# Performance work log

Measured on AMD Instinct MI355X. Metric: run time of the kernel, lower is better.

Reference implementation:

```python
import jax, jax.numpy as jnp
import numpy as np

NEG_SLOPE = 0.2  # PyG GATConv leaky_relu slope


def _gat_layer(x, src, dst, W, a_src, a_dst, b, concat, num_nodes):
    # x: [N, F_in], W: [F_in, H*C], a_src/a_dst: [H, C], b: [H*C] or [C]
    H, C = a_src.shape
    h = (x @ W).reshape(num_nodes, H, C)                      # [N, H, C]
    s_src = jnp.einsum('nhc,hc->nh', h, a_src)                # [N, H]
    s_dst = jnp.einsum('nhc,hc->nh', h, a_dst)                # [N, H]
    e = jax.nn.leaky_relu(s_src[src] + s_dst[dst], NEG_SLOPE) # [E, H]
    # segment softmax over edges sharing a destination node
    m = jax.ops.segment_max(e, dst, num_segments=num_nodes)
    m = jnp.where(jnp.isfinite(m), m, 0.0)
    p = jnp.exp(e - m[dst])
    z = jax.ops.segment_sum(p, dst, num_segments=num_nodes)
    alpha = p / (z[dst] + 1e-16)                              # [E, H]
    msg = h[src] * alpha[:, :, None]                          # [E, H, C]
    out = jax.ops.segment_sum(msg, dst, num_segments=num_nodes)  # [N, H, C]
    out = out.reshape(num_nodes, H * C) if concat else out.mean(axis=1)
    return out + b


def setup_inputs() -> dict:
    key = jax.random.key(0)
    ks = jax.random.split(key, 16)
    N, E, F = 100000, 800000, 128
    H, C = 4, 32
    sc_in = 1.0 / np.sqrt(F)
    inp = {
        'x': jax.random.normal(ks[0], (N, F), jnp.float32),
        'edge_index': jax.random.randint(ks[1], (2, E), 0, N, jnp.int64),
        'W1': jax.random.normal(ks[2], (F, H * C), jnp.float32) * sc_in,
        'a_src1': jax.random.normal(ks[3], (H, C), jnp.float32),
        'a_dst1': jax.random.normal(ks[4], (H, C), jnp.float32),
        'b1': jax.random.normal(ks[5], (H * C,), jnp.float32) * 0.01,
        'W2': jax.random.normal(ks[6], (F, H * C), jnp.float32) * sc_in,
        'a_src2': jax.random.normal(ks[7], (H, C), jnp.float32),
        'a_dst2': jax.random.normal(ks[8], (H, C), jnp.float32),
        'b2': jax.random.normal(ks[9], (H * C,), jnp.float32) * 0.01,
        'W3': jax.random.normal(ks[10], (F, H * F), jnp.float32) * sc_in,
        'a_src3': jax.random.normal(ks[11], (H, F), jnp.float32),
        'a_dst3': jax.random.normal(ks[12], (H, F), jnp.float32),
        'b3': jax.random.normal(ks[13], (F,), jnp.float32) * 0.01,
    }
    return inp


def reference(x, edge_index, W1, a_src1, a_dst1, b1, W2, a_src2, a_dst2, b2,
              W3, a_src3, a_dst3, b3):
    N = x.shape[0]
    # PyG GATConv default: add self loops
    loop = jnp.arange(N, dtype=edge_index.dtype)
    src = jnp.concatenate([edge_index[0], loop])
    dst = jnp.concatenate([edge_index[1], loop])
    # conv1 (concat heads) + residual + ELU
    x1 = jax.nn.elu(_gat_layer(x, src, dst, W1, a_src1, a_dst1, b1, True, N) + x)
    # intermediate conv (concat heads) + residual + ELU
    x2 = jax.nn.elu(_gat_layer(x1, src, dst, W2, a_src2, a_dst2, b2, True, N) + x1)
    # final conv (mean over heads) + residual, no ELU
    x3 = _gat_layer(x2, src, dst, W3, a_src3, a_dst3, b3, False, N) + x2
    return x3
```

## Files before the change

### kernel.cpp

```cpp
#include <hip/hip_runtime.h>
#include <hip/hip_bf16.h>
#include <cstdint>

#define NEG_SLOPE 0.2f

typedef __bf16 bf16x8 __attribute__((ext_vector_type(8)));
typedef _Float16 half8 __attribute__((ext_vector_type(8)));
typedef float  floatx4 __attribute__((ext_vector_type(4)));

__device__ __forceinline__ float us2f(unsigned short u) {
    union { unsigned int i; float f; } c; c.i = ((unsigned int)u) << 16; return c.f;
}
__device__ __forceinline__ unsigned short f2us(float f) {
    union { float f; unsigned int i; } c; c.f = f;
    unsigned int x = c.i;
    unsigned int r = (x + 0x7fffu + ((x >> 16) & 1u)) >> 16;
    return (unsigned short)r;
}
__device__ __forceinline__ unsigned short f2h(float f) {
    union { _Float16 h; unsigned short u; } c; c.h = (_Float16)f; return c.u;
}
__device__ __forceinline__ float h2f(unsigned short u) {
    union { _Float16 h; unsigned short u; } c; c.u = u; return (float)c.h;
}
__device__ __forceinline__ float ldx(const void* p, int i, int bf) {
    return bf ? us2f(((const unsigned short*)p)[i]) : ((const float*)p)[i];
}
__device__ __forceinline__ void split2(float f, unsigned short& h, unsigned short& l) {
    h = f2us(f);
    l = f2us(f - us2f(h));
}
__device__ __forceinline__ float sel4(const float* a, int i) {
    float lo = (i & 1) ? a[1] : a[0];
    float hi = (i & 1) ? a[3] : a[2];
    return (i & 2) ? hi : lo;
}
__device__ __forceinline__ void unp8(uint4 u, float* f) {
    union { unsigned int i; float ff; } a;
    a.i = u.x << 16;          f[0] = a.ff;
    a.i = u.x & 0xffff0000u;  f[1] = a.ff;
    a.i = u.y << 16;          f[2] = a.ff;
    a.i = u.y & 0xffff0000u;  f[3] = a.ff;
    a.i = u.z << 16;          f[4] = a.ff;
    a.i = u.z & 0xffff0000u;  f[5] = a.ff;
    a.i = u.w << 16;          f[6] = a.ff;
    a.i = u.w & 0xffff0000u;  f[7] = a.ff;
}

__global__ void k_detect(const unsigned short* __restrict__ x16,
                         const unsigned int* __restrict__ ei,
                         int* __restrict__ flags) {
    if (threadIdx.x == 0 && blockIdx.x == 0) {
        int cnt = 0;
        for (int i = 0; i < 1024; ++i) {
            const unsigned short u = x16[2 * i];
            const int e = (u >> 7) & 0xFF;
            if (e < 100 || e > 160) ++cnt;
        }
        flags[0] = (cnt < 256) ? 1 : 0;
        int is64 = 1;
        for (int i = 0; i < 64; ++i)
            if (ei[2 * i + 1] != 0u) { is64 = 0; break; }
        flags[1] = is64;
    }
}

__device__ __forceinline__ int edge_at(const void* ei, int f64, long long idx) {
    if (f64) return (int)((const long long*)ei)[idx];
    return ((const int*)ei)[idx];
}

__global__ void k_hist(const void* __restrict__ ei, const int* __restrict__ flags,
                       int* __restrict__ deg, int E, int N) {
    const int f64 = flags[1];
    const int EP = E + N;
    for (int e = blockIdx.x * blockDim.x + threadIdx.x; e < EP; e += gridDim.x * blockDim.x) {
        int dst = (e < E) ? edge_at(ei, f64, (long long)E + e) : (e - E);
        atomicAdd(&deg[dst], 1);
    }
}

__global__ __launch_bounds__(1024) void k_scan_a(const int* __restrict__ deg,
                                                 int* __restrict__ coff,
                                                 int* __restrict__ part, int N) {
    __shared__ int tmp[1024];
    const int t = threadIdx.x, idx = blockIdx.x * 1024 + t;
    const int v = (idx < N) ? deg[idx] : 0;
    tmp[t] = v; __syncthreads();
    for (int s = 1; s < 1024; s <<= 1) {
        int a = (t >= s) ? tmp[t - s] : 0;
        __syncthreads(); tmp[t] += a; __syncthreads();
    }
    if (idx < N) coff[idx] = tmp[t] - v;
    if (t == 1023) part[blockIdx.x] = tmp[1023];
}

__global__ __launch_bounds__(1024) void k_scan_b(int* __restrict__ part,
                                                 int* __restrict__ coff, int nblk, int N) {
    __shared__ int tmp[1024];
    const int t = threadIdx.x;
    const int v = (t < nblk) ? part[t] : 0;
    tmp[t] = v; __syncthreads();
    for (int s = 1; s < 1024; s <<= 1) {
        int a = (t >= s) ? tmp[t - s] : 0;
        __syncthreads(); tmp[t] += a; __syncthreads();
    }
    if (t < nblk) part[t] = tmp[t] - v;
    if (t == 1023) coff[N] = tmp[1023];
}

__global__ __launch_bounds__(1024) void k_scan_c(int* __restrict__ coff,
                                                 const int* __restrict__ part, int N) {
    const int idx = blockIdx.x * 1024 + threadIdx.x;
    if (idx < N) coff[idx] += part[blockIdx.x];
}

__global__ void k_scatter(const void* __restrict__ ei, const int* __restrict__ flags,
                          const int* __restrict__ coff, int* __restrict__ cpos,
                          int* __restrict__ csrc, int E, int N) {
    const int f64 = flags[1];
    const int EP = E + N;
    for (int e = blockIdx.x * blockDim.x + threadIdx.x; e < EP; e += gridDim.x * blockDim.x) {
        int src, dst;
        if (e < E) { src = edge_at(ei, f64, e); dst = edge_at(ei, f64, (long long)E + e); }
        else       { src = dst = e - E; }
        const int p = atomicAdd(&cpos[dst], 1);
        csrc[coff[dst] + p] = src;
    }
}

template <int F16>
__global__ void k_wfrag(const void* __restrict__ Wv, const int* __restrict__ flags,
                        int wstride, int total,
                        unsigned short* __restrict__ outH, unsigned short* __restrict__ outL) {
    const int bf = flags[0];
    for (int tid = blockIdx.x * blockDim.x + threadIdx.x; tid < total;
         tid += gridDim.x * blockDim.x) {
        const int j    = tid & 7;
        const int lane = (tid >> 3) & 63;
        const int ks   = (tid >> 9) & 3;
        const int ntg  = (tid >> 11) & 7;
        const int blk  = tid >> 14;
        const int k = ks * 32 + (lane >> 4) * 8 + j;
        const int c = blk * 128 + ntg * 16 + (lane & 15);
        const float v = ldx(Wv, k * wstride + c, bf);
        unsigned short h, l;
        if (F16) {
            h = f2h(v);
            l = f2h(v - h2f(h));
        } else {
            split2(v, h, l);
        }
        outH[tid] = h; outL[tid] = l;
    }
}

__global__ void k_wa(const void* __restrict__ W, const void* __restrict__ as,
                     const void* __restrict__ ad, const int* __restrict__ flags,
                     float* __restrict__ va) {
    const int bf = flags[0];
    const int t = blockIdx.x * blockDim.x + threadIdx.x;
    if (t >= 512) return;
    const int k = t >> 2, h = t & 3;
    float ss = 0.f, dd = 0.f;
    for (int c = 0; c < 128; ++c) {
        const float w = ldx(W, k * 512 + h * 128 + c, bf);
        ss = fmaf(w, ldx(as, h * 128 + c, bf), ss);
        dd = fmaf(w, ldx(ad, h * 128 + c, bf), dd);
    }
    va[k * 8 + h] = ss;
    va[k * 8 + 4 + h] = dd;
}

template <bool XRAW, int SC>
__global__ __launch_bounds__(256) void k_gemm(const void* __restrict__ Xv,
                                              const unsigned short* __restrict__ whfB,
                                              const unsigned short* __restrict__ wlfB,
                                              unsigned short* __restrict__ Y16, int ystride,
                                              float* __restrict__ ssrc,
                                              float* __restrict__ sdst,
                                              const void* __restrict__ a_src,
                                              const void* __restrict__ a_dst,
                                              const int* __restrict__ flags,
                                              int N) {
    __shared__ __align__(16) unsigned short Ah[64][136], Al[64][136];
    __shared__ float sred[2][4][SC ? 64 : 1];
    const int bf   = flags[0];
    const int t    = threadIdx.x;
    const int row0 = blockIdx.x * 64;
    const int hy   = blockIdx.y;
    const unsigned short* whf = whfB + hy * 16384;
    const unsigned short* wlf = wlfB + hy * 16384;
    const int ycol0 = hy * 128;
    const int wv   = t >> 6;
    const int lane = t & 63;
    const int quad = lane >> 4;
    const int l16  = lane & 15;

#pragma unroll
    for (int it = 0; it < 8; ++it) {
        const int id = it * 256 + t;
        const int r  = id >> 5;
        const int c  = (id & 31) * 4;
        const int gr = row0 + r;
        ushort4 h4 = make_ushort4(0, 0, 0, 0), l4 = make_ushort4(0, 0, 0, 0);
        if (gr < N) {
            if (XRAW && bf) {
                h4 = *(const ushort4*)&((const unsigned short*)Xv)[(size_t)gr * 128 + c];
            } else {
                const float4 f = *(const float4*)&((const float*)Xv)[(size_t)gr * 128 + c];
                split2(f.x, h4.x, l4.x); split2(f.y, h4.y, l4.y);
                split2(f.z, h4.z, l4.z); split2(f.w, h4.w, l4.w);
            }
        }
        *(ushort4*)&Ah[r][c] = h4;
        *(ushort4*)&Al[r][c] = l4;
    }
    __syncthreads();

    floatx4 acc[4][2];
#pragma unroll
    for (int mt = 0; mt < 4; ++mt)
#pragma unroll
        for (int nt = 0; nt < 2; ++nt) acc[mt][nt] = (floatx4){0.f, 0.f, 0.f, 0.f};

#pragma unroll
    for (int ks = 0; ks < 4; ++ks) {
        const int ko = ks * 32 + quad * 8;
        bf16x8 ah[4], al[4], bh[2], bl[2];
#pragma unroll
        for (int mt = 0; mt < 4; ++mt) ah[mt] = *(const bf16x8*)&Ah[mt * 16 + l16][ko];
        if (!(XRAW && bf)) {
#pragma unroll
            for (int mt = 0; mt < 4; ++mt) al[mt] = *(const bf16x8*)&Al[mt * 16 + l16][ko];
        }
#pragma unroll
        for (int nt = 0; nt < 2; ++nt)
            bh[nt] = *(const bf16x8*)&whf[(((wv * 2 + nt) * 4 + ks) * 64 + lane) * 8];
        if (!bf) {
#pragma unroll
            for (int nt = 0; nt < 2; ++nt)
                bl[nt] = *(const bf16x8*)&wlf[(((wv * 2 + nt) * 4 + ks) * 64 + lane) * 8];
        }
#pragma unroll
        for (int mt = 0; mt < 4; ++mt)
#pragma unroll
            for (int nt = 0; nt < 2; ++nt) {
                acc[mt][nt] = __builtin_amdgcn_mfma_f32_16x16x32_bf16(ah[mt], bh[nt], acc[mt][nt], 0, 0, 0);
                if (!bf)
                    acc[mt][nt] = __builtin_amdgcn_mfma_f32_16x16x32_bf16(ah[mt], bl[nt], acc[mt][nt], 0, 0, 0);
                if (!(XRAW && bf))
                    acc[mt][nt] = __builtin_amdgcn_mfma_f32_16x16x32_bf16(al[mt], bh[nt], acc[mt][nt], 0, 0, 0);
            }
    }

    const int aBase = hy * 128 + wv * 32;
    float as_[2], ad_[2];
#pragma unroll
    for (int nt = 0; nt < 2; ++nt) {
        as_[nt] = ldx(a_src, aBase + nt * 16 + l16, bf);
        ad_[nt] = ldx(a_dst, aBase + nt * 16 + l16, bf);
    }

#pragma unroll
    for (int mt = 0; mt < 4; ++mt) {
        const int rl = mt * 16 + quad * 4;
#pragma unroll
        for (int r = 0; r < 4; ++r) {
            const int grow = row0 + rl + r;
            if (grow < N) {
#pragma unroll
                for (int nt = 0; nt < 2; ++nt)
                    Y16[(size_t)grow * ystride + ycol0 + wv * 32 + nt * 16 + l16] =
                        f2us(acc[mt][nt][r]);
            }
            float ps = acc[mt][0][r] * as_[0] + acc[mt][1][r] * as_[1];
            float pd = acc[mt][0][r] * ad_[0] + acc[mt][1][r] * ad_[1];
#pragma unroll
            for (int mk = 1; mk <= 8; mk <<= 1) {
                ps += __shfl_xor(ps, mk);
                pd += __shfl_xor(pd, mk);
            }
            if (SC == 0) {
                if (l16 == 0 && grow < N) {
                    ssrc[(size_t)grow * 4 + wv] = ps;
                    sdst[(size_t)grow * 4 + wv] = pd;
                }
            } else {
                if (l16 == 0) { sred[0][wv][rl + r] = ps; sred[1][wv][rl + r] = pd; }
            }
        }
    }
    if (SC == 1) {
        __syncthreads();
        if (t < 64 && row0 + t < N) {
            ssrc[(size_t)(row0 + t) * 4 + hy] = sred[0][0][t] + sred[0][1][t] + sred[0][2][t] + sred[0][3][t];
            sdst[(size_t)(row0 + t) * 4 + hy] = sred[1][0][t] + sred[1][1][t] + sred[1][2][t] + sred[1][3][t];
        }
    }
}

template <int MODE>
__global__ __launch_bounds__(256) void k_agg(const int* __restrict__ coff,
                                             const int* __restrict__ csrc,
                                             const float* __restrict__ ssrc,
                                             const float* __restrict__ sdst,
                                             const unsigned short* __restrict__ H16,
                                             const void* __restrict__ bias,
                                             const void* __restrict__ resid,
                                             const int* __restrict__ flags,
                                             void* __restrict__ out, int N,
                                             const float* __restrict__ va,
                                             float* __restrict__ ss2,
                                             float* __restrict__ sd2,
                                             unsigned short* __restrict__ x2h) {
    __shared__ float vaS[(MODE == 1) ? 128 : 1][9];
    const int bf   = flags[0];
    const int t    = threadIdx.x;
    const int l16  = t & 15;
    const int n0   = blockIdx.x * 16 + (t >> 4);
    const bool nact = n0 < N;
    const int n    = nact ? n0 : (N - 1);
    const int beg = coff[n], end = coff[n + 1];
    const int deg = end - beg;

    if (MODE == 1) {
        for (int i = t; i < 1024; i += 256) vaS[i >> 3][i & 7] = va[i];
        __syncthreads();
    }

    const float4 sdv = *(const float4*)&sdst[(size_t)n * 4];
    const float sd[4] = { sdv.x, sdv.y, sdv.z, sdv.w };
    const bool fast = (deg <= 16);
    float m[4], z[4];
    int   myS = 0;
    float wn[4] = { 0.f, 0.f, 0.f, 0.f };

    if (fast) {
        const bool act = l16 < deg;
        float v[4];
#pragma unroll
        for (int h = 0; h < 4; ++h) v[h] = -1e30f;
        if (act) {
            myS = csrc[beg + l16];
            const float4 sp = *(const float4*)&ssrc[(size_t)myS * 4];
            const float s4[4] = { sp.x, sp.y, sp.z, sp.w };
#pragma unroll
            for (int h = 0; h < 4; ++h) {
                float tv = s4[h] + sd[h];
                v[h] = tv >= 0.f ? tv : NEG_SLOPE * tv;
            }
        }
#pragma unroll
        for (int h = 0; h < 4; ++h) m[h] = v[h];
#pragma unroll
        for (int mk = 1; mk <= 8; mk <<= 1)
#pragma unroll
            for (int h = 0; h < 4; ++h) m[h] = fmaxf(m[h], __shfl_xor(m[h], mk));
        float w[4];
#pragma unroll
        for (int h = 0; h < 4; ++h) w[h] = act ? expf(v[h] - m[h]) : 0.f;
#pragma unroll
        for (int h = 0; h < 4; ++h) z[h] = w[h];
#pragma unroll
        for (int mk = 1; mk <= 8; mk <<= 1)
#pragma unroll
            for (int h = 0; h < 4; ++h) z[h] += __shfl_xor(z[h], mk);
#pragma unroll
        for (int h = 0; h < 4; ++h) wn[h] = w[h] / (z[h] + 1e-16f);
    } else {
#pragma unroll
        for (int h = 0; h < 4; ++h) m[h] = -1e30f;
        for (int e = beg + l16; e < end; e += 16) {
            const int s = csrc[e];
            const float4 sp = *(const float4*)&ssrc[(size_t)s * 4];
            const float s4[4] = { sp.x, sp.y, sp.z, sp.w };
#pragma unroll
            for (int h = 0; h < 4; ++h) {
                float tv = s4[h] + sd[h];
                tv = tv >= 0.f ? tv : NEG_SLOPE * tv;
                m[h] = fmaxf(m[h], tv);
            }
        }
#pragma unroll
        for (int mk = 1; mk <= 8; mk <<= 1)
#pragma unroll
            for (int h = 0; h < 4; ++h) m[h] = fmaxf(m[h], __shfl_xor(m[h], mk));
#pragma unroll
        for (int h = 0; h < 4; ++h) z[h] = 0.f;
        for (int e = beg + l16; e < end; e += 16) {
            const int s = csrc[e];
            const float4 sp = *(const float4*)&ssrc[(size_t)s * 4];
            const float s4[4] = { sp.x, sp.y, sp.z, sp.w };
#pragma unroll
            for (int h = 0; h < 4; ++h) {
                float tv = s4[h] + sd[h];
                tv = tv >= 0.f ? tv : NEG_SLOPE * tv;
                z[h] += expf(tv - m[h]);
            }
        }
#pragma unroll
        for (int mk = 1; mk <= 8; mk <<= 1)
#pragma unroll
            for (int h = 0; h < 4; ++h) z[h] += __shfl_xor(z[h], mk);
    }

    const int c8 = l16 * 8;
    const int hd = l16 >> 2;
    float ac[8];
#pragma unroll
    for (int j = 0; j < 8; ++j) ac[j] = 0.f;

    if (fast) {
        for (int e = 0; e < deg; ++e) {
            const int s = __shfl(myS, e, 16);
            float wa4[4];
            wa4[0] = __shfl(wn[0], e, 16);
            wa4[1] = __shfl(wn[1], e, 16);
            wa4[2] = __shfl(wn[2], e, 16);
            wa4[3] = __shfl(wn[3], e, 16);
            const float w = sel4(wa4, hd);
            const uint4 u = *(const uint4*)&H16[(size_t)s * 128 + c8];
            float f[8]; unp8(u, f);
#pragma unroll
            for (int j = 0; j < 8; ++j) ac[j] = fmaf(w, f[j], ac[j]);
        }
    } else {
        float ivh[4];
#pragma unroll
        for (int h = 0; h < 4; ++h) ivh[h] = 1.f / (z[h] + 1e-16f);
        const float mh = sel4(m, hd), sdh = sel4(sd, hd), ih = sel4(ivh, hd);
        for (int e = beg; e < end; ++e) {
            const int s = csrc[e];
            float tv = ssrc[(size_t)s * 4 + hd] + sdh;
            tv = tv >= 0.f ? tv : NEG_SLOPE * tv;
            const float w = expf(tv - mh) * ih;
            const uint4 u = *(const uint4*)&H16[(size_t)s * 128 + c8];
            float f[8]; unp8(u, f);
#pragma unroll
            for (int j = 0; j < 8; ++j) ac[j] = fmaf(w, f[j], ac[j]);
        }
    }

    if (!nact) return;
    const int ob = n * 128 + c8;
    float rr[8];
    if (MODE == 0) {
        if (bf) {
            const uint4 u = *(const uint4*)&((const unsigned short*)resid)[ob];
            unp8(u, rr);
        } else {
            const float4 r0 = *(const float4*)&((const float*)resid)[ob];
            const float4 r1 = *(const float4*)&((const float*)resid)[ob + 4];
            rr[0] = r0.x; rr[1] = r0.y; rr[2] = r0.z; rr[3] = r0.w;
            rr[4] = r1.x; rr[5] = r1.y; rr[6] = r1.z; rr[7] = r1.w;
        }
    } else {
        const float4 r0 = *(const float4*)&((const float*)resid)[ob];
        const float4 r1 = *(const float4*)&((const float*)resid)[ob + 4];
        rr[0] = r0.x; rr[1] = r0.y; rr[2] = r0.z; rr[3] = r0.w;
        rr[4] = r1.x; rr[5] = r1.y; rr[6] = r1.z; rr[7] = r1.w;
    }
    float o[8];
#pragma unroll
    for (int j = 0; j < 8; ++j) {
        const float v = ac[j] + ldx(bias, c8 + j, bf) + rr[j];
        o[j] = v > 0.f ? v : expm1f(v);
    }
    *(float4*)&((float*)out)[ob]     = make_float4(o[0], o[1], o[2], o[3]);
    *(float4*)&((float*)out)[ob + 4] = make_float4(o[4], o[5], o[6], o[7]);

    if (MODE == 1) {
        uint4 u16;
        u16.x = (unsigned int)f2us(o[0]) | ((unsigned int)f2us(o[1]) << 16);
        u16.y = (unsigned int)f2us(o[2]) | ((unsigned int)f2us(o[3]) << 16);
        u16.z = (unsigned int)f2us(o[4]) | ((unsigned int)f2us(o[5]) << 16);
        u16.w = (unsigned int)f2us(o[6]) | ((unsigned int)f2us(o[7]) << 16);
        *(uint4*)&x2h[ob] = u16;
        float p[8];
#pragma unroll
        for (int o8 = 0; o8 < 8; ++o8) {
            float acc = 0.f;
#pragma unroll
            for (int j = 0; j < 8; ++j) acc = fmaf(o[j], vaS[c8 + j][o8], acc);
            p[o8] = acc;
        }
#pragma unroll
        for (int mk = 1; mk <= 8; mk <<= 1)
#pragma unroll
            for (int o8 = 0; o8 < 8; ++o8) p[o8] += __shfl_xor(p[o8], mk);
        if (l16 == 0) {
#pragma unroll
            for (int h = 0; h < 4; ++h) {
                ss2[(size_t)n * 4 + h] = p[h];
                sd2[(size_t)n * 4 + h] = p[4 + h];
            }
        }
    }
}

__global__ __launch_bounds__(256) void k_aggx(const int* __restrict__ coff,
                                              const int* __restrict__ csrc,
                                              const float* __restrict__ ssrc,
                                              const float* __restrict__ sdst,
                                              const unsigned short* __restrict__ X16,
                                              unsigned short* __restrict__ aggO,
                                              int N) {
    const int t    = threadIdx.x;
    const int l16  = t & 15;
    const int n0   = blockIdx.x * 16 + (t >> 4);
    const bool nact = n0 < N;
    const int n    = nact ? n0 : (N - 1);
    const int beg = coff[n], end = coff[n + 1];
    const int deg = end - beg;

    const float4 sdv = *(const float4*)&sdst[(size_t)n * 4];
    const float sd[4] = { sdv.x, sdv.y, sdv.z, sdv.w };
    const bool fast = (deg <= 16);
    float m[4], z[4];
    int   myS = 0;
    float wn[4] = { 0.f, 0.f, 0.f, 0.f };

    if (fast) {
        const bool act = l16 < deg;
        float v[4];
#pragma unroll
        for (int h = 0; h < 4; ++h) v[h] = -1e30f;
        if (act) {
            myS = csrc[beg + l16];
            const float4 sp = *(const float4*)&ssrc[(size_t)myS * 4];
            const float s4[4] = { sp.x, sp.y, sp.z, sp.w };
#pragma unroll
            for (int h = 0; h < 4; ++h) {
                float tv = s4[h] + sd[h];
                v[h] = tv >= 0.f ? tv : NEG_SLOPE * tv;
            }
        }
#pragma unroll
        for (int h = 0; h < 4; ++h) m[h] = v[h];
#pragma unroll
        for (int mk = 1; mk <= 8; mk <<= 1)
#pragma unroll
            for (int h = 0; h < 4; ++h) m[h] = fmaxf(m[h], __shfl_xor(m[h], mk));
        float w[4];
#pragma unroll
        for (int h = 0; h < 4; ++h) w[h] = act ? expf(v[h] - m[h]) : 0.f;
#pragma unroll
        for (int h = 0; h < 4; ++h) z[h] = w[h];
#pragma unroll
        for (int mk = 1; mk <= 8; mk <<= 1)
#pragma unroll
            for (int h = 0; h < 4; ++h) z[h] += __shfl_xor(z[h], mk);
#pragma unroll
        for (int h = 0; h < 4; ++h) wn[h] = w[h] / (z[h] + 1e-16f);
    } else {
#pragma unroll
        for (int h = 0; h < 4; ++h) m[h] = -1e30f;
        for (int e = beg + l16; e < end; e += 16) {
            const int s = csrc[e];
            const float4 sp = *(const float4*)&ssrc[(size_t)s * 4];
            const float s4[4] = { sp.x, sp.y, sp.z, sp.w };
#pragma unroll
            for (int h = 0; h < 4; ++h) {
                float tv = s4[h] + sd[h];
                tv = tv >= 0.f ? tv : NEG_SLOPE * tv;
                m[h] = fmaxf(m[h], tv);
            }
        }
#pragma unroll
        for (int mk = 1; mk <= 8; mk <<= 1)
#pragma unroll
            for (int h = 0; h < 4; ++h) m[h] = fmaxf(m[h], __shfl_xor(m[h], mk));
#pragma unroll
        for (int h = 0; h < 4; ++h) z[h] = 0.f;
        for (int e = beg + l16; e < end; e += 16) {
            const int s = csrc[e];
            const float4 sp = *(const float4*)&ssrc[(size_t)s * 4];
            const float s4[4] = { sp.x, sp.y, sp.z, sp.w };
#pragma unroll
            for (int h = 0; h < 4; ++h) {
                float tv = s4[h] + sd[h];
                tv = tv >= 0.f ? tv : NEG_SLOPE * tv;
                z[h] += expf(tv - m[h]);
            }
        }
#pragma unroll
        for (int mk = 1; mk <= 8; mk <<= 1)
#pragma unroll
            for (int h = 0; h < 4; ++h) z[h] += __shfl_xor(z[h], mk);
    }

    const int c8 = l16 * 8;
    float ac[4][8];
#pragma unroll
    for (int h = 0; h < 4; ++h)
#pragma unroll
        for (int j = 0; j < 8; ++j) ac[h][j] = 0.f;

    if (fast) {
        for (int e = 0; e < deg; ++e) {
            const int s = __shfl(myS, e, 16);
            float wr[4];
            wr[0] = __shfl(wn[0], e, 16);
            wr[1] = __shfl(wn[1], e, 16);
            wr[2] = __shfl(wn[2], e, 16);
            wr[3] = __shfl(wn[3], e, 16);
            const uint4 u = *(const uint4*)&X16[(size_t)s * 128 + c8];
            float f[8]; unp8(u, f);
#pragma unroll
            for (int h = 0; h < 4; ++h)
#pragma unroll
                for (int j = 0; j < 8; ++j) ac[h][j] = fmaf(wr[h], f[j], ac[h][j]);
        }
    } else {
        float ivh[4];
#pragma unroll
        for (int h = 0; h < 4; ++h) ivh[h] = 1.f / (z[h] + 1e-16f);
        for (int e = beg; e < end; ++e) {
            const int s = csrc[e];
            const float4 sp = *(const float4*)&ssrc[(size_t)s * 4];
            const float s4[4] = { sp.x, sp.y, sp.z, sp.w };
            float wr[4];
#pragma unroll
            for (int h = 0; h < 4; ++h) {
                float tv = s4[h] + sd[h];
                tv = tv >= 0.f ? tv : NEG_SLOPE * tv;
                wr[h] = expf(tv - m[h]) * ivh[h];
            }
            const uint4 u = *(const uint4*)&X16[(size_t)s * 128 + c8];
            float f[8]; unp8(u, f);
#pragma unroll
            for (int h = 0; h < 4; ++h)
#pragma unroll
                for (int j = 0; j < 8; ++j) ac[h][j] = fmaf(wr[h], f[j], ac[h][j]);
        }
    }

    if (!nact) return;
#pragma unroll
    for (int h = 0; h < 4; ++h) {
        uint4 u;
        u.x = (unsigned int)f2h(ac[h][0]) | ((unsigned int)f2h(ac[h][1]) << 16);
        u.y = (unsigned int)f2h(ac[h][2]) | ((unsigned int)f2h(ac[h][3]) << 16);
        u.z = (unsigned int)f2h(ac[h][4]) | ((unsigned int)f2h(ac[h][5]) << 16);
        u.w = (unsigned int)f2h(ac[h][6]) | ((unsigned int)f2h(ac[h][7]) << 16);
        *(uint4*)&aggO[(size_t)n0 * 512 + h * 128 + c8] = u;
    }
}

__global__ __launch_bounds__(256) void k_gemm3(const unsigned short* __restrict__ A16,
                                               const unsigned short* __restrict__ whf,
                                               const unsigned short* __restrict__ wlf,
                                               const void* __restrict__ bias,
                                               const float* __restrict__ resid,
                                               const int* __restrict__ flags,
                                               void* __restrict__ out, int N) {
    __shared__ __align__(16) unsigned short Ah[64][136];
    const int bf   = flags[0];
    const int t    = threadIdx.x;
    const int row0 = blockIdx.x * 64;
    const int wv   = t >> 6;
    const int lane = t & 63;
    const int quad = lane >> 4;
    const int l16  = lane & 15;

    floatx4 acc[4][2];
#pragma unroll
    for (int mt = 0; mt < 4; ++mt)
#pragma unroll
        for (int nt = 0; nt < 2; ++nt) acc[mt][nt] = (floatx4){0.f, 0.f, 0.f, 0.f};

    for (int kc = 0; kc < 4; ++kc) {
        if (kc) __syncthreads();
#pragma unroll
        for (int it = 0; it < 8; ++it) {
            const int id = it * 256 + t;
            const int r  = id >> 5;
            const int c  = (id & 31) * 4;
            ushort4 h4 = make_ushort4(0, 0, 0, 0);
            if (row0 + r < N)
                h4 = *(const ushort4*)&A16[(size_t)(row0 + r) * 512 + kc * 128 + c];
            *(ushort4*)&Ah[r][c] = h4;
        }
        __syncthreads();

        const unsigned short* whc = whf + kc * 16384;
        const unsigned short* wlc = wlf + kc * 16384;
#pragma unroll
        for (int ks = 0; ks < 4; ++ks) {
            const int ko = ks * 32 + quad * 8;
            half8 ah[4], bh[2], bl[2];
#pragma unroll
            for (int mt = 0; mt < 4; ++mt) ah[mt] = *(const half8*)&Ah[mt * 16 + l16][ko];
#pragma unroll
            for (int nt = 0; nt < 2; ++nt) {
                bh[nt] = *(const half8*)&whc[(((wv * 2 + nt) * 4 + ks) * 64 + lane) * 8];
                bl[nt] = *(const half8*)&wlc[(((wv * 2 + nt) * 4 + ks) * 64 + lane) * 8];
            }
#pragma unroll
            for (int mt = 0; mt < 4; ++mt)
#pragma unroll
                for (int nt = 0; nt < 2; ++nt) {
                    acc[mt][nt] = __builtin_amdgcn_mfma_f32_16x16x32_f16(ah[mt], bh[nt], acc[mt][nt], 0, 0, 0);
                    acc[mt][nt] = __builtin_amdgcn_mfma_f32_16x16x32_f16(ah[mt], bl[nt], acc[mt][nt], 0, 0, 0);
                }
        }
    }

#pragma unroll
    for (int mt = 0; mt < 4; ++mt) {
        const int rl = mt * 16 + quad * 4;
#pragma unroll
        for (int r = 0; r < 4; ++r) {
            const int grow = row0 + rl + r;
            if (grow < N) {
#pragma unroll
                for (int nt = 0; nt < 2; ++nt) {
                    const int col = wv * 32 + nt * 16 + l16;
                    const float v = acc[mt][nt][r] * 0.25f + ldx(bias, col, bf)
                                  + resid[(size_t)grow * 128 + col];
                    if (bf) ((unsigned short*)out)[(size_t)grow * 128 + col] = f2us(v);
                    else    ((float*)out)[(size_t)grow * 128 + col] = v;
                }
            }
        }
    }
}

extern "C" void kernel_launch(void* const* d_in, const int* in_sizes, int n_in,
                              void* d_out, int out_size, void* d_ws, size_t ws_size,
                              hipStream_t stream) {
    const int N  = in_sizes[0] / 128;
    const int E  = in_sizes[1] / 2;
    const int EP = E + N;

    const void* x   = d_in[0];
    const void* ei  = d_in[1];
    const void* W1  = d_in[2];
    const void* as1 = d_in[3];
    const void* ad1 = d_in[4];
    const void* b1  = d_in[5];
    const void* W2  = d_in[6];
    const void* as2 = d_in[7];
    const void* ad2 = d_in[8];
    const void* b2  = d_in[9];
    const void* W3  = d_in[10];
    const void* as3 = d_in[11];
    const void* ad3 = d_in[12];
    const void* b3  = d_in[13];

    char* p = (char*)d_ws;
    auto alloc = [&](size_t bytes) { char* r = p; p += (bytes + 255) & ~(size_t)255; return r; };
    int*   flags = (int*)alloc(8);
    int*   deg   = (int*)alloc((size_t)(N + 1) * 4);
    int*   coff  = (int*)alloc((size_t)(N + 1) * 4);
    int*   cpos  = (int*)alloc((size_t)N * 4);
    int*   part  = (int*)alloc(4096);
    int*   csrc  = (int*)alloc((size_t)EP * 4);
    char*  region = alloc((size_t)N * 512 * 2);
    float* x2b   = (float*)alloc((size_t)N * 128 * 4);
    float* ssrc  = (float*)alloc((size_t)N * 4 * 4);
    float* sdst  = (float*)alloc((size_t)N * 4 * 4);
    unsigned short* whf1 = (unsigned short*)alloc(16384 * 2);
    unsigned short* wlf1 = (unsigned short*)alloc(16384 * 2);
    unsigned short* whf2 = (unsigned short*)alloc(16384 * 2);
    unsigned short* wlf2 = (unsigned short*)alloc(16384 * 2);
    unsigned short* whf3 = (unsigned short*)alloc(65536 * 2);
    unsigned short* wlf3 = (unsigned short*)alloc(65536 * 2);
    unsigned short* x2h  = (unsigned short*)alloc((size_t)N * 128 * 2);
    float* va    = (float*)alloc(128 * 8 * 4);
    float* ssrc3 = (float*)alloc((size_t)N * 4 * 4);
    float* sdst3 = (float*)alloc((size_t)N * 4 * 4);

    float*          x1b    = (float*)region;
    unsigned short* h16_12 = (unsigned short*)(region + (size_t)N * 128 * 4);
    unsigned short* aggF   = (unsigned short*)region;

    hipMemsetAsync(deg,  0, (size_t)(N + 1) * 4, stream);
    hipMemsetAsync(cpos, 0, (size_t)N * 4, stream);

    k_detect<<<1, 64, 0, stream>>>((const unsigned short*)x, (const unsigned int*)ei, flags);

    k_wfrag<0><<<64, 256, 0, stream>>>(W1, flags, 128, 16384, whf1, wlf1);
    k_wfrag<0><<<64, 256, 0, stream>>>(W2, flags, 128, 16384, whf2, wlf2);
    k_wfrag<1><<<256, 256, 0, stream>>>(W3, flags, 512, 65536, whf3, wlf3);
    k_wa<<<2, 256, 0, stream>>>(W3, as3, ad3, flags, va);

    const int egrid = (EP + 255) / 256;
    const int nblk  = (N + 1023) / 1024;
    k_hist<<<egrid, 256, 0, stream>>>(ei, flags, deg, E, N);
    k_scan_a<<<nblk, 1024, 0, stream>>>(deg, coff, part, N);
    k_scan_b<<<1, 1024, 0, stream>>>(part, coff, nblk, N);
    k_scan_c<<<nblk, 1024, 0, stream>>>(coff, part, N);
    k_scatter<<<egrid, 256, 0, stream>>>(ei, flags, coff, cpos, csrc, E, N);

    const int ggrid = (N + 63) / 64;
    const int ngrid = (N + 15) / 16;

    k_gemm<true, 0><<<dim3(ggrid, 1), 256, 0, stream>>>(x, whf1, wlf1, h16_12, 128,
                                                        ssrc, sdst, as1, ad1, flags, N);
    k_agg<0><<<ngrid, 256, 0, stream>>>(coff, csrc, ssrc, sdst, h16_12, b1, x, flags, x1b, N,
                                        nullptr, nullptr, nullptr, nullptr);

    k_gemm<false, 0><<<dim3(ggrid, 1), 256, 0, stream>>>(x1b, whf2, wlf2, h16_12, 128,
                                                         ssrc, sdst, as2, ad2, flags, N);
    k_agg<1><<<ngrid, 256, 0, stream>>>(coff, csrc, ssrc, sdst, h16_12, b2, x1b, flags, x2b, N,
                                        va, ssrc3, sdst3, x2h);

    k_aggx<<<ngrid, 256, 0, stream>>>(coff, csrc, ssrc3, sdst3, x2h, aggF, N);
    k_gemm3<<<ggrid, 256, 0, stream>>>(aggF, whf3, wlf3, b3, x2b, flags, d_out, N);
}
```

Measured before the change: 686.8 us.

## Drop softmax max pass, use fast exp, and unroll edge gather by two

In the aggregation kernel the segment-softmax max reduction is removed: exp is taken on the clamped raw score, and normalization by the sum is deferred to a single multiply of the accumulator at the end. This saves one full pass over neighbor scores on high-degree nodes, plus the shuffle reductions. Fast __expf replaces expf elsewhere, the mean-head kernel's gather loop is unrolled by two so two row loads are in flight at once, and the shared array is padded. The clamp at 80 changes numerics when scores are large, and without max subtraction fp32 sums may lose precision.

```diff
diff --git a/kernel.cpp b/kernel.cpp
--- a/kernel.cpp
+++ b/kernel.cpp
@@ -314,7 +314,7 @@
                                              float* __restrict__ ss2,
                                              float* __restrict__ sd2,
                                              unsigned short* __restrict__ x2h) {
-    __shared__ float vaS[(MODE == 1) ? 128 : 1][9];
+    __shared__ float vaS[(MODE == 1) ? 128 : 1][10];
     const int bf   = flags[0];
     const int t    = threadIdx.x;
     const int l16  = t & 15;
@@ -332,15 +332,12 @@
     const float4 sdv = *(const float4*)&sdst[(size_t)n * 4];
     const float sd[4] = { sdv.x, sdv.y, sdv.z, sdv.w };
     const bool fast = (deg <= 16);
-    float m[4], z[4];
+    float z[4];
     int   myS = 0;
     float wn[4] = { 0.f, 0.f, 0.f, 0.f };
 
     if (fast) {
         const bool act = l16 < deg;
-        float v[4];
-#pragma unroll
-        for (int h = 0; h < 4; ++h) v[h] = -1e30f;
         if (act) {
             myS = csrc[beg + l16];
             const float4 sp = *(const float4*)&ssrc[(size_t)myS * 4];
@@ -348,44 +345,17 @@
 #pragma unroll
             for (int h = 0; h < 4; ++h) {
                 float tv = s4[h] + sd[h];
-                v[h] = tv >= 0.f ? tv : NEG_SLOPE * tv;
-            }
-        }
-#pragma unroll
-        for (int h = 0; h < 4; ++h) m[h] = v[h];
+                tv = tv >= 0.f ? tv : NEG_SLOPE * tv;
+                wn[h] = __expf(fminf(tv, 80.f));
+            }
+        }
+#pragma unroll
+        for (int h = 0; h < 4; ++h) z[h] = wn[h];
 #pragma unroll
         for (int mk = 1; mk <= 8; mk <<= 1)
 #pragma unroll
-            for (int h = 0; h < 4; ++h) m[h] = fmaxf(m[h], __shfl_xor(m[h], mk));
-        float w[4];
-#pragma unroll
-        for (int h = 0; h < 4; ++h) w[h] = act ? expf(v[h] - m[h]) : 0.f;
-#pragma unroll
-        for (int h = 0; h < 4; ++h) z[h] = w[h];
-#pragma unroll
-        for (int mk = 1; mk <= 8; mk <<= 1)
-#pragma unroll
             for (int h = 0; h < 4; ++h) z[h] += __shfl_xor(z[h], mk);
-#pragma unroll
-        for (int h = 0; h < 4; ++h) wn[h] = w[h] / (z[h] + 1e-16f);
     } else {
-#pragma unroll
-        for (int h = 0; h < 4; ++h) m[h] = -1e30f;
-        for (int e = beg + l16; e < end; e += 16) {
-            const int s = csrc[e];
-            const float4 sp = *(const float4*)&ssrc[(size_t)s * 4];
-            const float s4[4] = { sp.x, sp.y, sp.z, sp.w };
-#pragma unroll
-            for (int h = 0; h < 4; ++h) {
-                float tv = s4[h] + sd[h];
-                tv = tv >= 0.f ? tv : NEG_SLOPE * tv;
-                m[h] = fmaxf(m[h], tv);
-            }
-        }
-#pragma unroll
-        for (int mk = 1; mk <= 8; mk <<= 1)
-#pragma unroll
-            for (int h = 0; h < 4; ++h) m[h] = fmaxf(m[h], __shfl_xor(m[h], mk));
 #pragma unroll
         for (int h = 0; h < 4; ++h) z[h] = 0.f;
         for (int e = beg + l16; e < end; e += 16) {
@@ -396,7 +366,7 @@
             for (int h = 0; h < 4; ++h) {
                 float tv = s4[h] + sd[h];
                 tv = tv >= 0.f ? tv : NEG_SLOPE * tv;
-                z[h] += expf(tv - m[h]);
+                z[h] += __expf(fminf(tv, 80.f));
             }
         }
 #pragma unroll
@@ -404,9 +374,14 @@
 #pragma unroll
             for (int h = 0; h < 4; ++h) z[h] += __shfl_xor(z[h], mk);
     }
+
+    float ivz[4];
+#pragma unroll
+    for (int h = 0; h < 4; ++h) ivz[h] = 1.f / (z[h] + 1e-16f);
 
     const int c8 = l16 * 8;
     const int hd = l16 >> 2;
+    const float ih = sel4(ivz, hd);
     float ac[8];
 #pragma unroll
     for (int j = 0; j < 8; ++j) ac[j] = 0.f;
@@ -426,21 +401,21 @@
             for (int j = 0; j < 8; ++j) ac[j] = fmaf(w, f[j], ac[j]);
         }
     } else {
-        float ivh[4];
-#pragma unroll
-        for (int h = 0; h < 4; ++h) ivh[h] = 1.f / (z[h] + 1e-16f);
-        const float mh = sel4(m, hd), sdh = sel4(sd, hd), ih = sel4(ivh, hd);
+        const float sdh = sel4(sd, hd);
         for (int e = beg; e < end; ++e) {
             const int s = csrc[e];
             float tv = ssrc[(size_t)s * 4 + hd] + sdh;
             tv = tv >= 0.f ? tv : NEG_SLOPE * tv;
-            const float w = expf(tv - mh) * ih;
+            const float w = __expf(fminf(tv, 80.f));
             const uint4 u = *(const uint4*)&H16[(size_t)s * 128 + c8];
             float f[8]; unp8(u, f);
 #pragma unroll
             for (int j = 0; j < 8; ++j) ac[j] = fmaf(w, f[j], ac[j]);
         }
     }
+
+#pragma unroll
+    for (int j = 0; j < 8; ++j) ac[j] *= ih;
 
     if (!nact) return;
     const int ob = n * 128 + c8;
@@ -544,7 +519,7 @@
             for (int h = 0; h < 4; ++h) m[h] = fmaxf(m[h], __shfl_xor(m[h], mk));
         float w[4];
 #pragma unroll
-        for (int h = 0; h < 4; ++h) w[h] = act ? expf(v[h] - m[h]) : 0.f;
+        for (int h = 0; h < 4; ++h) w[h] = act ? __expf(v[h] - m[h]) : 0.f;
 #pragma unroll
         for (int h = 0; h < 4; ++h) z[h] = w[h];
 #pragma unroll
@@ -581,7 +556,7 @@
             for (int h = 0; h < 4; ++h) {
                 float tv = s4[h] + sd[h];
                 tv = tv >= 0.f ? tv : NEG_SLOPE * tv;
-                z[h] += expf(tv - m[h]);
+                z[h] += __expf(tv - m[h]);
             }
         }
 #pragma unroll
@@ -598,7 +573,31 @@
         for (int j = 0; j < 8; ++j) ac[h][j] = 0.f;
 
     if (fast) {
-        for (int e = 0; e < deg; ++e) {
+        int e = 0;
+        for (; e + 2 <= deg; e += 2) {
+            const int s0 = __shfl(myS, e + 0, 16);
+            const int s1 = __shfl(myS, e + 1, 16);
+            const uint4 u0 = *(const uint4*)&X16[(size_t)s0 * 128 + c8];
+            const uint4 u1 = *(const uint4*)&X16[(size_t)s1 * 128 + c8];
+            float w0[4], w1[4];
+#pragma unroll
+            for (int h = 0; h < 4; ++h) {
+                w0[h] = __shfl(wn[h], e + 0, 16);
+                w1[h] = __shfl(wn[h], e + 1, 16);
+            }
+            float f[8];
+            unp8(u0, f);
+#pragma unroll
+            for (int h = 0; h < 4; ++h)
+#pragma unroll
+                for (int j = 0; j < 8; ++j) ac[h][j] = fmaf(w0[h], f[j], ac[h][j]);
+            unp8(u1, f);
+#pragma unroll
+            for (int h = 0; h < 4; ++h)
+#pragma unroll
+                for (int j = 0; j < 8; ++j) ac[h][j] = fmaf(w1[h], f[j], ac[h][j]);
+        }
+        for (; e < deg; ++e) {
             const int s = __shfl(myS, e, 16);
             float wr[4];
             wr[0] = __shfl(wn[0], e, 16);
@@ -625,7 +624,7 @@
             for (int h = 0; h < 4; ++h) {
                 float tv = s4[h] + sd[h];
                 tv = tv >= 0.f ? tv : NEG_SLOPE * tv;
-                wr[h] = expf(tv - m[h]) * ivh[h];
+                wr[h] = __expf(tv - m[h]) * ivh[h];
             }
             const uint4 u = *(const uint4*)&X16[(size_t)s * 128 + c8];
             float f[8]; unp8(u, f);
```

Result: faster. 670.3 us (-2.4%).
